# Kernel optimization log

Hardware: AMD Instinct MI355X
Metric: run time of the kernel (lower is better)

Reference implementation:

```python
import jax, jax.numpy as jnp
import numpy as np

EPS = 1e-15
MAX_TANH_ARG = 1.0 - 1e-5  # clamp for artanh domain, standard in Poincare-ball libs


def logmap0(x):
    # Poincare ball, c=1: logmap0(x) = artanh(||x||) * x / ||x||
    norm = jnp.linalg.norm(x, axis=-1, keepdims=True)
    norm_c = jnp.clip(norm, EPS, MAX_TANH_ARG)
    scale = jnp.arctanh(norm_c) / jnp.maximum(norm, EPS)
    return scale * x


def expmap0(v):
    # Poincare ball, c=1: expmap0(v) = tanh(||v||) * v / ||v||
    norm = jnp.linalg.norm(v, axis=-1, keepdims=True)
    scale = jnp.tanh(norm) / jnp.maximum(norm, EPS)
    return scale * v


def setup_inputs() -> dict:
    key = jax.random.key(0)
    k1, k2, k3, k4 = jax.random.split(key, 4)
    N, E, D_IN, D_OUT = 50000, 600000, 128, 128
    # points loosely inside/near the ball; logmap0 clamps the norm anyway
    x = jax.random.uniform(k1, (N, D_IN), dtype=jnp.float32)
    edge_index = jax.random.randint(k2, (2, E), 0, N, dtype=jnp.int32)
    W = jax.random.normal(k3, (D_OUT, D_IN), dtype=jnp.float32) / np.sqrt(D_IN)
    b = jax.random.normal(k4, (D_OUT,), dtype=jnp.float32) * 0.01
    return {"x": x, "edge_index": edge_index, "W": W, "b": b}


def reference(x, edge_index, W, b):
    num_nodes = x.shape[0]
    src, dst = edge_index[0], edge_index[1]

    x_tangent = logmap0(x)                       # [N, D_in]
    h = x_tangent @ W.T + b                      # [N, D_out]

    # symmetric degree count: each edge adds 1 to dst and 1 to src
    ones = jnp.ones(src.shape[0], dtype=jnp.float32)
    deg = (jax.ops.segment_sum(ones, dst, num_segments=num_nodes)
           + jax.ops.segment_sum(ones, src, num_segments=num_nodes))
    deg = jnp.maximum(deg, 1.0)
    dinv = deg ** -0.5                           # [N]

    # fused gather-scale-scatter across ALL feature dims at once
    msg = h[src] * (dinv[src] * dinv[dst])[:, None]   # [E, D_out]
    out = jax.ops.segment_sum(msg, dst, num_segments=num_nodes)  # [N, D_out]

    return expmap0(out)
```

## Files before the change

kernel.cpp:

```cpp
#include <hip/hip_runtime.h>
#include <math.h>

#define D 128
#define CAP 48

typedef __attribute__((ext_vector_type(8))) short short8;
typedef __attribute__((ext_vector_type(4))) float f32x4;

__device__ inline unsigned short f2bf(float f) {
  unsigned int u = __float_as_uint(f);
  u = (u + 0x7FFFu + ((u >> 16) & 1u)) >> 16;
  return (unsigned short)u;
}
__device__ inline float bf2f(unsigned int us) {
  return __uint_as_float(us << 16);
}

__global__ __launch_bounds__(256) void k_fused(
    const float* __restrict__ x, const float* __restrict__ W,
    const float* __restrict__ b, const int* __restrict__ src,
    const int* __restrict__ dst, int* __restrict__ indeg,
    int* __restrict__ outdeg, int* __restrict__ ebuf,
    unsigned short* __restrict__ h, int N, int E, int ET) {
  __shared__ unsigned short Wl[16 * 128 * 8];
  __shared__ float bs[D];

  const int t = threadIdx.x;
  const int w = t >> 6;
  const int l = t & 63;

  for (int i = t * 4; i < D * D; i += 1024) {
    float4 wv = *(const float4*)(W + i);
    int r = i >> 7, c = i & 127;
    int idx = ((c >> 3) << 10) + (r << 3) + (c & 7);
    ushort4 pk = make_ushort4(f2bf(wv.x), f2bf(wv.y), f2bf(wv.z), f2bf(wv.w));
    *(ushort4*)(&Wl[idx]) = pk;
  }
  if (t < D) bs[t] = b[t];
  __syncthreads();

  if (w >= 2) {
    int et = blockIdx.x * 128 + (t - 128);
    for (int e = et; e < E; e += ET) {
      int d = dst[e], s = src[e];
      int pos = atomicAdd(&indeg[d], 1);
      if (pos < CAP) ebuf[(size_t)d * CAP + pos] = s;
      atomicAdd(&outdeg[s], 1);
    }
    return;
  }

  const int lc = l & 15;
  const int q = l >> 4;
  const int r0 = blockIdx.x * 32;
  const int grow = r0 + w * 16 + lc;
  const bool ok = grow < N;
  const float* xp = x + (size_t)grow * D + q * 8;

  short8 a[4];
  float ss = 0.0f;
#pragma unroll
  for (int kk = 0; kk < 4; ++kk) {
    float4 u = ok ? *(const float4*)(xp + kk * 32) : make_float4(0, 0, 0, 0);
    float4 v = ok ? *(const float4*)(xp + kk * 32 + 4) : make_float4(0, 0, 0, 0);
    ss += u.x * u.x + u.y * u.y + u.z * u.z + u.w * u.w;
    ss += v.x * v.x + v.y * v.y + v.z * v.z + v.w * v.w;
    short8 af;
    af[0] = (short)f2bf(u.x); af[1] = (short)f2bf(u.y);
    af[2] = (short)f2bf(u.z); af[3] = (short)f2bf(u.w);
    af[4] = (short)f2bf(v.x); af[5] = (short)f2bf(v.y);
    af[6] = (short)f2bf(v.z); af[7] = (short)f2bf(v.w);
    a[kk] = af;
  }
  ss += __shfl_xor(ss, 16, 64);
  ss += __shfl_xor(ss, 32, 64);
  float nrm = sqrtf(ss);
  float nc = fminf(fmaxf(nrm, 1e-15f), 1.0f - 1e-5f);
  float rs = atanhf(nc) / fmaxf(nrm, 1e-15f);

  f32x4 acc[8];
#pragma unroll
  for (int nt = 0; nt < 8; ++nt) acc[nt] = (f32x4){0.f, 0.f, 0.f, 0.f};

#pragma unroll
  for (int kk = 0; kk < 4; ++kk) {
#pragma unroll
    for (int nt = 0; nt < 8; ++nt) {
      short8 bf = *(const short8*)(&Wl[((kk * 4 + q) << 10) + ((nt * 16 + lc) << 3)]);
      acc[nt] = __builtin_amdgcn_mfma_f32_16x16x32_bf16(a[kk], bf, acc[nt], 0, 0, 0);
    }
  }

  float rsl[4];
#pragma unroll
  for (int i = 0; i < 4; ++i) rsl[i] = __shfl(rs, q * 4 + i, 64);

#pragma unroll
  for (int nt = 0; nt < 8; ++nt) {
    int j = nt * 16 + lc;
    float bj = bs[j];
#pragma unroll
    for (int i = 0; i < 4; ++i) {
      int gr = r0 + w * 16 + q * 4 + i;
      if (gr < N) h[(size_t)gr * D + j] = f2bf(rsl[i] * acc[nt][i] + bj);
    }
  }
}

__global__ __launch_bounds__(256) void k_dinv(const int* __restrict__ indeg,
                                              const int* __restrict__ outdeg,
                                              float* __restrict__ dinv, int N) {
  int i = blockIdx.x * 256 + threadIdx.x;
  if (i < N) dinv[i] = rsqrtf(fmaxf((float)(indeg[i] + outdeg[i]), 1.0f));
}

__global__ __launch_bounds__(256) void k_gather_expmap(
    const unsigned short* __restrict__ h, const int* __restrict__ ebuf,
    const int* __restrict__ indeg, const float* __restrict__ dinv,
    float* __restrict__ out, int N) {
  int gid = blockIdx.x * 256 + threadIdx.x;
  int r = gid >> 6, lane = gid & 63;
  if (r >= N) return;

  int cnt = indeg[r];
  if (cnt > CAP) cnt = CAP;
  const int* eb = ebuf + (size_t)r * CAP;

  int s_l = (lane < cnt) ? eb[lane] : 0;
  float dv_l = (lane < cnt) ? dinv[s_l] : 0.0f;

  const int half = lane >> 5;
  const int m = lane & 31;

  float a0 = 0.f, a1 = 0.f, a2 = 0.f, a3 = 0.f;
  for (int i = 0; i < cnt; i += 4) {
    int e0 = i + half, e1 = i + 2 + half;
    int sA = __shfl(s_l, e0, 64);
    int sB = __shfl(s_l, e1, 64);
    float wA = __shfl(dv_l, e0, 64);
    float wB = __shfl(dv_l, e1, 64);
    wA = (e0 < cnt) ? wA : 0.0f;
    wB = (e1 < cnt) ? wB : 0.0f;
    uint2 pA = *(const uint2*)(h + (size_t)sA * D + m * 4);
    uint2 pB = *(const uint2*)(h + (size_t)sB * D + m * 4);
    a0 += wA * bf2f(pA.x & 0xFFFFu);
    a1 += wA * bf2f(pA.x >> 16);
    a2 += wA * bf2f(pA.y & 0xFFFFu);
    a3 += wA * bf2f(pA.y >> 16);
    a0 += wB * bf2f(pB.x & 0xFFFFu);
    a1 += wB * bf2f(pB.x >> 16);
    a2 += wB * bf2f(pB.y & 0xFFFFu);
    a3 += wB * bf2f(pB.y >> 16);
  }

  a0 += __shfl_xor(a0, 32, 64);
  a1 += __shfl_xor(a1, 32, 64);
  a2 += __shfl_xor(a2, 32, 64);
  a3 += __shfl_xor(a3, 32, 64);

  float di_d = dinv[r];
  a0 *= di_d; a1 *= di_d; a2 *= di_d; a3 *= di_d;

  float sN = a0 * a0 + a1 * a1 + a2 * a2 + a3 * a3;
#pragma unroll
  for (int off = 1; off < 32; off <<= 1) sN += __shfl_xor(sN, off, 64);
  float n = sqrtf(sN);
  float sc = tanhf(n) / fmaxf(n, 1e-15f);

  if (lane < 32) {
    float4 o = make_float4(a0 * sc, a1 * sc, a2 * sc, a3 * sc);
    *(float4*)(out + (size_t)r * D + m * 4) = o;
  }
}

extern "C" void kernel_launch(void* const* d_in, const int* in_sizes, int n_in,
                              void* d_out, int out_size, void* d_ws, size_t ws_size,
                              hipStream_t stream) {
  const float* x = (const float*)d_in[0];
  const int* ei = (const int*)d_in[1];
  const float* W = (const float*)d_in[2];
  const float* b = (const float*)d_in[3];
  float* out = (float*)d_out;

  const int N = in_sizes[0] / D;
  const int E = in_sizes[1] / 2;
  const int* src = ei;
  const int* dst = ei + E;

  unsigned short* h = (unsigned short*)d_ws;
  float* dinv = (float*)(h + (size_t)N * D);
  int* indeg = (int*)(dinv + N);
  int* outdeg = indeg + N;
  int* ebuf = outdeg + N;

  hipMemsetAsync(indeg, 0, (size_t)N * 2 * sizeof(int), stream);

  const int NB = (N + 31) / 32;
  const int ET = NB * 128;
  k_fused<<<NB, 256, 0, stream>>>(x, W, b, src, dst, indeg, outdeg, ebuf, h, N, E, ET);
  k_dinv<<<(N + 255) / 256, 256, 0, stream>>>(indeg, outdeg, dinv, N);
  k_gather_expmap<<<(int)(((long long)N * 64 + 255) / 256), 256, 0, stream>>>(
      h, ebuf, indeg, dinv, out, N);
}
```

Measured before the change: 166.5 us.

## Pack in/out degrees into one counter, drop dinv kernel, widen gather unroll

In-degree and out-degree are now packed into one 32-bit counter: the low 16 bits count incoming edges and the high 16 bits count outgoing ones. This halves the memset and lets the gather kernel compute the normalisation factors inline, so the separate dinv kernel launch goes away. The gather loop now has each of the 64 lanes handle two features of a row and issues 8 neighbor loads per iteration instead of 2 per half-wave, to raise memory-level parallelism. Risks are counter overflow past 65535 per node and more padded loads against row 0 when the neighbor count is not a multiple of 8.

```diff
diff --git a/kernel.cpp b/kernel.cpp
--- a/kernel.cpp
+++ b/kernel.cpp
@@ -19,9 +19,9 @@
 __global__ __launch_bounds__(256) void k_fused(
     const float* __restrict__ x, const float* __restrict__ W,
     const float* __restrict__ b, const int* __restrict__ src,
-    const int* __restrict__ dst, int* __restrict__ indeg,
-    int* __restrict__ outdeg, int* __restrict__ ebuf,
-    unsigned short* __restrict__ h, int N, int E, int ET) {
+    const int* __restrict__ dst, unsigned int* __restrict__ deg,
+    int* __restrict__ ebuf, unsigned short* __restrict__ h, int N, int E,
+    int ET) {
   __shared__ unsigned short Wl[16 * 128 * 8];
   __shared__ float bs[D];
 
@@ -33,19 +33,18 @@
     float4 wv = *(const float4*)(W + i);
     int r = i >> 7, c = i & 127;
     int idx = ((c >> 3) << 10) + (r << 3) + (c & 7);
-    ushort4 pk = make_ushort4(f2bf(wv.x), f2bf(wv.y), f2bf(wv.z), f2bf(wv.w));
-    *(ushort4*)(&Wl[idx]) = pk;
+    *(ushort4*)(&Wl[idx]) =
+        make_ushort4(f2bf(wv.x), f2bf(wv.y), f2bf(wv.z), f2bf(wv.w));
   }
   if (t < D) bs[t] = b[t];
   __syncthreads();
 
   if (w >= 2) {
-    int et = blockIdx.x * 128 + (t - 128);
-    for (int e = et; e < E; e += ET) {
+    for (int e = blockIdx.x * 128 + (t - 128); e < E; e += ET) {
       int d = dst[e], s = src[e];
-      int pos = atomicAdd(&indeg[d], 1);
+      unsigned int pos = atomicAdd(&deg[d], 1u) & 0xFFFFu;
       if (pos < CAP) ebuf[(size_t)d * CAP + pos] = s;
-      atomicAdd(&outdeg[s], 1);
+      atomicAdd(&deg[s], 0x10000u);
     }
     return;
   }
@@ -107,70 +106,53 @@
   }
 }
 
-__global__ __launch_bounds__(256) void k_dinv(const int* __restrict__ indeg,
-                                              const int* __restrict__ outdeg,
-                                              float* __restrict__ dinv, int N) {
-  int i = blockIdx.x * 256 + threadIdx.x;
-  if (i < N) dinv[i] = rsqrtf(fmaxf((float)(indeg[i] + outdeg[i]), 1.0f));
-}
-
-__global__ __launch_bounds__(256) void k_gather_expmap(
+__global__ __launch_bounds__(256) void k_gather(
     const unsigned short* __restrict__ h, const int* __restrict__ ebuf,
-    const int* __restrict__ indeg, const float* __restrict__ dinv,
-    float* __restrict__ out, int N) {
+    const unsigned int* __restrict__ deg, float* __restrict__ out, int N) {
   int gid = blockIdx.x * 256 + threadIdx.x;
-  int r = gid >> 6, lane = gid & 63;
+  int r = gid >> 6, l = gid & 63;
   if (r >= N) return;
 
-  int cnt = indeg[r];
+  unsigned int vr = deg[r];
+  int cnt = (int)(vr & 0xFFFFu);
   if (cnt > CAP) cnt = CAP;
+  float di_d = rsqrtf(fmaxf((float)((vr & 0xFFFFu) + (vr >> 16)), 1.0f));
   const int* eb = ebuf + (size_t)r * CAP;
 
-  int s_l = (lane < cnt) ? eb[lane] : 0;
-  float dv_l = (lane < cnt) ? dinv[s_l] : 0.0f;
+  int s_l = (l < cnt) ? eb[l] : 0;
+  unsigned int vs = (l < cnt) ? deg[s_l] : 0u;
+  float dv_l =
+      (l < cnt) ? rsqrtf(fmaxf((float)((vs & 0xFFFFu) + (vs >> 16)), 1.0f)) : 0.0f;
 
-  const int half = lane >> 5;
-  const int m = lane & 31;
-
-  float a0 = 0.f, a1 = 0.f, a2 = 0.f, a3 = 0.f;
-  for (int i = 0; i < cnt; i += 4) {
-    int e0 = i + half, e1 = i + 2 + half;
-    int sA = __shfl(s_l, e0, 64);
-    int sB = __shfl(s_l, e1, 64);
-    float wA = __shfl(dv_l, e0, 64);
-    float wB = __shfl(dv_l, e1, 64);
-    wA = (e0 < cnt) ? wA : 0.0f;
-    wB = (e1 < cnt) ? wB : 0.0f;
-    uint2 pA = *(const uint2*)(h + (size_t)sA * D + m * 4);
-    uint2 pB = *(const uint2*)(h + (size_t)sB * D + m * 4);
-    a0 += wA * bf2f(pA.x & 0xFFFFu);
-    a1 += wA * bf2f(pA.x >> 16);
-    a2 += wA * bf2f(pA.y & 0xFFFFu);
-    a3 += wA * bf2f(pA.y >> 16);
-    a0 += wB * bf2f(pB.x & 0xFFFFu);
-    a1 += wB * bf2f(pB.x >> 16);
-    a2 += wB * bf2f(pB.y & 0xFFFFu);
-    a3 += wB * bf2f(pB.y >> 16);
+  float ax = 0.0f, ay = 0.0f;
+  for (int i = 0; i < cnt; i += 8) {
+    unsigned int pv[8];
+    float wj[8];
+#pragma unroll
+    for (int j = 0; j < 8; ++j) {
+      int s = __shfl(s_l, i + j, 64);
+      wj[j] = __shfl(dv_l, i + j, 64);
+      pv[j] = *(const unsigned int*)(h + (size_t)s * D + l * 2);
+    }
+#pragma unroll
+    for (int j = 0; j < 8; ++j) {
+      ax += wj[j] * bf2f(pv[j] & 0xFFFFu);
+      ay += wj[j] * bf2f(pv[j] >> 16);
+    }
   }
 
-  a0 += __shfl_xor(a0, 32, 64);
-  a1 += __shfl_xor(a1, 32, 64);
-  a2 += __shfl_xor(a2, 32, 64);
-  a3 += __shfl_xor(a3, 32, 64);
+  ax *= di_d;
+  ay *= di_d;
 
-  float di_d = dinv[r];
-  a0 *= di_d; a1 *= di_d; a2 *= di_d; a3 *= di_d;
-
-  float sN = a0 * a0 + a1 * a1 + a2 * a2 + a3 * a3;
+  float sN = ax * ax + ay * ay;
 #pragma unroll
-  for (int off = 1; off < 32; off <<= 1) sN += __shfl_xor(sN, off, 64);
+  for (int off = 32; off > 0; off >>= 1) sN += __shfl_down(sN, off, 64);
+  sN = __shfl(sN, 0, 64);
   float n = sqrtf(sN);
   float sc = tanhf(n) / fmaxf(n, 1e-15f);
 
-  if (lane < 32) {
-    float4 o = make_float4(a0 * sc, a1 * sc, a2 * sc, a3 * sc);
-    *(float4*)(out + (size_t)r * D + m * 4) = o;
-  }
+  float2* op = (float2*)(out + (size_t)r * D);
+  op[l] = make_float2(ax * sc, ay * sc);
 }
 
 extern "C" void kernel_launch(void* const* d_in, const int* in_sizes, int n_in,
@@ -188,17 +170,14 @@
   const int* dst = ei + E;
 
   unsigned short* h = (unsigned short*)d_ws;
-  float* dinv = (float*)(h + (size_t)N * D);
-  int* indeg = (int*)(dinv + N);
-  int* outdeg = indeg + N;
-  int* ebuf = outdeg + N;
+  unsigned int* deg = (unsigned int*)(h + (size_t)N * D);
+  int* ebuf = (int*)(deg + N);
 
-  hipMemsetAsync(indeg, 0, (size_t)N * 2 * sizeof(int), stream);
+  hipMemsetAsync(deg, 0, (size_t)N * sizeof(unsigned int), stream);
 
   const int NB = (N + 31) / 32;
   const int ET = NB * 128;
-  k_fused<<<NB, 256, 0, stream>>>(x, W, b, src, dst, indeg, outdeg, ebuf, h, N, E, ET);
-  k_dinv<<<(N + 255) / 256, 256, 0, stream>>>(indeg, outdeg, dinv, N);
-  k_gather_expmap<<<(int)(((long long)N * 64 + 255) / 256), 256, 0, stream>>>(
-      h, ebuf, indeg, dinv, out, N);
+  k_fused<<<NB, 256, 0, stream>>>(x, W, b, src, dst, deg, ebuf, h, N, E, ET);
+  k_gather<<<(int)(((long long)N * 64 + 255) / 256), 256, 0, stream>>>(
+      h, ebuf, deg, out, N);
 }
```

Result: no change. 164.8 us (-1.0%).
